# Kernel tuning notes

Hardware: AMD Instinct MI355X
Metric: run time of the kernel (lower is better)

## Reference

```python
import jax, jax.numpy as jnp
import numpy as np

B, S, L, E, H, T, V, D = 32, 256, 24, 300, 256, 16, 50000, 256  # batch, sents, words/sent, emb, gru_units, topics, vocab, dense


def setup_inputs() -> dict:
    key = jax.random.key(0)
    ks = jax.random.split(key, 12)
    word_ids = jax.random.randint(ks[0], (B, S, L), 0, V, dtype=jnp.int32)
    tsize = S // T
    starts = (jnp.arange(T, dtype=jnp.int32) * tsize + 1)          # 1-indexed inclusive
    ends = (jnp.arange(T, dtype=jnp.int32) * tsize + tsize)
    topic_start_ends = jnp.broadcast_to(jnp.stack([starts, ends], -1)[None], (B, T, 2))
    g = lambda k, shape, sc=0.05: (jax.random.normal(k, shape, jnp.float32) * sc)
    return {
        "word_ids": word_ids,
        "topic_start_ends": topic_start_ends,
        "emb": g(ks[1], (V, E), 0.1),
        "Wih_f": g(ks[2], (3 * H, E)), "Whh_f": g(ks[3], (3 * H, H)),
        "bih_f": jnp.zeros((3 * H,), jnp.float32), "bhh_f": jnp.zeros((3 * H,), jnp.float32),
        "Wih_b": g(ks[4], (3 * H, E)), "Whh_b": g(ks[5], (3 * H, H)),
        "bih_b": jnp.zeros((3 * H,), jnp.float32), "bhh_b": jnp.zeros((3 * H,), jnp.float32),
        "W_att": g(ks[6], (4 * H, 4 * H)), "v_att": g(ks[7], (4 * H, 1)),
        "W_dna": g(ks[8], (4 * H, D)), "b_dna": jnp.zeros((D,), jnp.float32),
        "W_out": g(ks[9], (D, 1)), "b_out": jnp.zeros((1,), jnp.float32),
    }


def _gru_dir(x, Wih, Whh, bih, bhh, reverse):
    # x: [B, S, E] -> outputs [B, S, H], final hidden [B, H]  (PyTorch GRU cell math)
    def step(h, xt):
        gi = xt @ Wih.T + bih
        gh = h @ Whh.T + bhh
        ir, iz, inn = jnp.split(gi, 3, axis=-1)
        hr, hz, hn = jnp.split(gh, 3, axis=-1)
        r = jax.nn.sigmoid(ir + hr)
        z = jax.nn.sigmoid(iz + hz)
        n = jnp.tanh(inn + r * hn)
        h2 = (1.0 - z) * n + z * h
        return h2, h2
    h0 = jnp.zeros((x.shape[0], Whh.shape[1]), x.dtype)
    hT, ys = jax.lax.scan(step, h0, jnp.swapaxes(x, 0, 1), reverse=reverse)
    return jnp.swapaxes(ys, 0, 1), hT


def _gather_seq(x, idx):
    # x: [B, S', C], idx: [B, K] -> [B, K, C]
    return jnp.take_along_axis(x, idx[:, :, None].astype(jnp.int32), axis=1)


def reference(word_ids, topic_start_ends, emb, Wih_f, Whh_f, bih_f, bhh_f,
              Wih_b, Whh_b, bih_b, bhh_b, W_att, v_att, W_dna, b_dna, W_out, b_out):
    # --- sent_encoder: per-sentence mean of word embeddings ---
    sent_vecs = jnp.mean(emb[word_ids], axis=2)  # [B, S, E]

    # --- doc_encoder: bidirectional GRU ---
    out_f, hT_f = _gru_dir(sent_vecs, Wih_f, Whh_f, bih_f, bhh_f, reverse=False)
    out_b, hT_b = _gru_dir(sent_vecs, Wih_b, Whh_b, bih_b, bhh_b, reverse=True)
    sent_rep = jnp.concatenate([out_f, out_b], axis=-1)          # [B, S, 2H]
    hidden = jnp.stack([hT_f, hT_b], axis=0)                     # [2, B, H]
    # faithful to torch: hidden.view(batch_size, 2H) (row-major reshape)
    doc_vec = hidden.reshape(B, 2 * H)
    doc_rep = jnp.broadcast_to(doc_vec[:, None, :], (B, S, 2 * H))

    # --- topic representation via boundary differencing on front/back-padded output ---
    padded = jnp.pad(sent_rep, ((0, 0), (1, 1), (0, 0)))         # [B, S+2, 2H]
    starts = topic_start_ends[..., 0]                            # [B, T], 1-indexed
    ends = topic_start_ends[..., 1]
    topic_fwd = _gather_seq(padded, ends)[..., :H] - _gather_seq(padded, starts - 1)[..., :H]
    topic_bwd = _gather_seq(padded, starts)[..., H:] - _gather_seq(padded, ends + 1)[..., H:]
    topic_mat = jnp.concatenate([topic_fwd, topic_bwd], axis=-1)  # [B, T, 2H]
    # sentence s (0-indexed) -> topic t with starts[t] <= s+1 <= ends[t]
    sent_1idx = jnp.arange(1, S + 1, dtype=jnp.int32)
    topic_id = jax.vmap(lambda e: jnp.searchsorted(e, sent_1idx, side='left'))(ends)  # [B, S]
    topic_rep = jnp.take_along_axis(topic_mat, topic_id[:, :, None], axis=1)          # [B, S, 2H]

    # --- decoder_attention ---
    cat_ds = jnp.concatenate([doc_rep, sent_rep], axis=-1)       # [B, S, 4H]
    cat_ts = jnp.concatenate([topic_rep, sent_rep], axis=-1)
    doc_scores = jnp.tanh(cat_ds @ W_att) @ v_att                # [B, S, 1]
    topic_scores = jnp.tanh(cat_ts @ W_att) @ v_att
    doc_w = jax.nn.softmax(doc_scores, axis=1)
    topic_w = jax.nn.softmax(topic_scores, axis=1)
    context = doc_w * doc_rep + topic_w * topic_rep              # [B, S, 2H]
    inp = jnp.concatenate([sent_rep, context], axis=-1)          # [B, S, 4H]
    h = jax.nn.relu(inp @ W_dna + b_dna)                         # dropout is identity (eval)
    logits = (h @ W_out + b_out)[..., 0]                         # [B, S]
    return logits
```

## Files before the change

kernel.cpp:

```cpp
#include <hip/hip_runtime.h>
#include <hip/hip_bf16.h>
#include <math.h>

#define Bd 32
#define Sd 256
#define Ld 24
#define Ed 300
#define Hd 256
#define Td 16
#define Dd 256
#define EP 320

using short8 = __attribute__((ext_vector_type(8))) short;
using f32x4  = __attribute__((ext_vector_type(4))) float;

__device__ __forceinline__ float fsigm(float x) { return 1.f / (1.f + __expf(-x)); }
__device__ __forceinline__ float ftanh(float x) {
  float e = __expf(2.f * x);
  return 1.f - 2.f / (e + 1.f);
}

__global__ void sent_means_kernel(const int* __restrict__ wids,
                                  const float* __restrict__ emb,
                                  __hip_bfloat16* __restrict__ apad) {
  int r = blockIdx.x;
  __shared__ int ids[Ld];
  int tid = threadIdx.x;
  if (tid < Ld) ids[tid] = wids[r * Ld + tid];
  __syncthreads();
  float acc = 0.f;
  if (tid < Ed) {
#pragma unroll
    for (int w = 0; w < Ld; ++w) acc += emb[(size_t)ids[w] * Ed + tid];
    acc *= (1.f / 24.f);
  }
  apad[r * EP + tid] = __float2bfloat16(tid < Ed ? acc : 0.f);
}

__global__ void prep1_kernel(const float* __restrict__ wih_f, const float* __restrict__ wih_b,
                             const float* __restrict__ whh_f, const float* __restrict__ whh_b,
                             __hip_bfloat16* __restrict__ wpadf, __hip_bfloat16* __restrict__ wpadb,
                             __hip_bfloat16* __restrict__ whhbf_f, __hip_bfloat16* __restrict__ whhbf_b) {
  int i = blockIdx.x * 512 + threadIdx.x;
  const int PW = 768 * EP;
  const int WH = 768 * Hd;
  if (i < 2 * PW) {
    const float* src = (i < PW) ? wih_f : wih_b;
    __hip_bfloat16* dst = (i < PW) ? wpadf : wpadb;
    int j = (i < PW) ? i : i - PW;
    int n = j / EP, k = j % EP;
    dst[j] = __float2bfloat16(k < Ed ? src[n * Ed + k] : 0.f);
  } else {
    int j = i - 2 * PW;
    const float* src = (j < WH) ? whh_f : whh_b;
    __hip_bfloat16* dst = (j < WH) ? whhbf_f : whhbf_b;
    int k = (j < WH) ? j : j - WH;
    dst[k] = __float2bfloat16(src[k]);
  }
}

__global__ __launch_bounds__(256) void gemm_xwt_kernel(
    const __hip_bfloat16* __restrict__ A, int lda,
    const __hip_bfloat16* __restrict__ W, int ldw,
    float* __restrict__ C, int ldc,
    int M, int N, int K,
    const float* __restrict__ bias) {
  __shared__ unsigned short la[64][32];
  __shared__ unsigned short lb[64][32];
  const int tid = threadIdx.x;
  const int m0 = blockIdx.x * 64, n0 = blockIdx.y * 64;
  const int lane = tid & 63, wid = tid >> 6;
  const int wm = (wid >> 1) * 32, wn = (wid & 1) * 32;
  const int lrow = tid >> 2, lcol = (tid & 3) * 8;
  f32x4 acc00 = {0.f, 0.f, 0.f, 0.f}, acc01 = {0.f, 0.f, 0.f, 0.f};
  f32x4 acc10 = {0.f, 0.f, 0.f, 0.f}, acc11 = {0.f, 0.f, 0.f, 0.f};
  int arow = m0 + lrow; if (arow > M - 1) arow = M - 1;
  const int brow = n0 + lrow;
  const int fr = lane & 15, fq = (lane >> 4) * 8;
  for (int k0 = 0; k0 < K; k0 += 32) {
    uint4 av = *(const uint4*)(A + (size_t)arow * lda + k0 + lcol);
    uint4 bv = *(const uint4*)(W + (size_t)brow * ldw + k0 + lcol);
    *(uint4*)(&la[lrow][lcol]) = av;
    *(uint4*)(&lb[lrow][lcol]) = bv;
    __syncthreads();
    short8 a0 = *(const short8*)(&la[wm + fr][fq]);
    short8 a1 = *(const short8*)(&la[wm + 16 + fr][fq]);
    short8 b0 = *(const short8*)(&lb[wn + fr][fq]);
    short8 b1 = *(const short8*)(&lb[wn + 16 + fr][fq]);
    acc00 = __builtin_amdgcn_mfma_f32_16x16x32_bf16(a0, b0, acc00, 0, 0, 0);
    acc01 = __builtin_amdgcn_mfma_f32_16x16x32_bf16(a0, b1, acc01, 0, 0, 0);
    acc10 = __builtin_amdgcn_mfma_f32_16x16x32_bf16(a1, b0, acc10, 0, 0, 0);
    acc11 = __builtin_amdgcn_mfma_f32_16x16x32_bf16(a1, b1, acc11, 0, 0, 0);
    __syncthreads();
  }
  const int rq = (lane >> 4) * 4;
  f32x4 accs[2][2] = {{acc00, acc01}, {acc10, acc11}};
  for (int i = 0; i < 2; ++i)
    for (int j = 0; j < 2; ++j) {
      int n = n0 + wn + j * 16 + fr;
      float bv = bias ? bias[n] : 0.f;
      for (int r2 = 0; r2 < 4; ++r2) {
        int m = m0 + wm + i * 16 + rq + r2;
        if (m < M) C[(size_t)m * ldc + n] = accs[i][j][r2] + bv;
      }
    }
}

__global__ __launch_bounds__(512, 2) void gru_mfma_kernel(
    const float* __restrict__ gi_f, const float* __restrict__ gi_b,
    const __hip_bfloat16* __restrict__ whhbf_f, const __hip_bfloat16* __restrict__ whhbf_b,
    const float* __restrict__ bhh_f, const float* __restrict__ bhh_b,
    float* __restrict__ sent_rep, __hip_bfloat16* __restrict__ sent_rep_bf,
    float* __restrict__ hT_f, float* __restrict__ hT_b,
    const float* __restrict__ w_att, const float* __restrict__ w_dna,
    __hip_bfloat16* __restrict__ wpack1, __hip_bfloat16* __restrict__ wpack2) {
  __shared__ float gi_lds[2][8][768];
  __shared__ __hip_bfloat16 h_bf[256];
  __shared__ float gh[768];
  __shared__ float stg32[8][256];
  const int blk = blockIdx.x;
  const int tid = threadIdx.x;

  if (blk >= 64) {
    const size_t q = (size_t)(blk - 64) * 512 + tid;
    size_t flat = q * 8;
    const size_t HALF = (size_t)1280 * 512;
    const bool second = flat >= HALF;
    size_t r = second ? flat - HALF : flat;
    int n = (int)(r >> 9), k0 = (int)(r & 511);
    __hip_bfloat16* dst = second ? wpack2 : wpack1;
#pragma unroll
    for (int j = 0; j < 8; ++j) {
      int k = k0 + j;
      float v;
      if (!second)
        v = (n < 1024) ? w_att[(size_t)k * 1024 + n]
                       : w_dna[(size_t)(512 + k) * 256 + (n - 1024)];
      else
        v = (n < 1024) ? w_att[(size_t)(512 + k) * 1024 + n]
                       : w_dna[(size_t)k * 256 + (n - 1024)];
      dst[(size_t)n * 512 + k] = __float2bfloat16(v);
    }
    return;
  }

  const int dir = blk >> 5, b = blk & 31;
  const int lane = tid & 63, w = tid >> 6;
  const float* gi = dir ? gi_b : gi_f;
  const __hip_bfloat16* whh = dir ? whhbf_b : whhbf_f;
  const float* bhh = dir ? bhh_b : bhh_f;

  if (tid < 256) h_bf[tid] = __float2bfloat16(0.f);

  short8 bfrag[6][8];
  {
    const int n0 = w * 96 + (lane & 15);
    const int kq = (lane >> 4) * 8;
#pragma unroll
    for (int nt = 0; nt < 6; ++nt)
#pragma unroll
      for (int kt = 0; kt < 8; ++kt)
        bfrag[nt][kt] = *(const short8*)(whh + (size_t)(n0 + nt * 16) * 256 + kt * 32 + kq);
  }
  float bhr = 0.f, bhz = 0.f, bhn = 0.f, hprev = 0.f;
  if (tid < 256) { bhr = bhh[tid]; bhz = bhh[256 + tid]; bhn = bhh[512 + tid]; }

  auto burst = [&](int tstart, int buf) {
#pragma unroll
    for (int i = 0; i < 3; ++i) {
      int idx = tid + i * 512;
      int u = idx / 192;
      int c4 = (idx - u * 192) * 4;
      int s = dir ? (255 - (tstart + u)) : (tstart + u);
      float4 v = *(const float4*)(gi + (size_t)(((b << 8) + s) * 768 + c4));
      *(float4*)(&gi_lds[buf][u][c4]) = v;
    }
  };
  burst(0, 0);
  __syncthreads();

  const int c = lane & 15;
  const int kq = (lane >> 4) * 8;
  const short8 zero8 = {0, 0, 0, 0, 0, 0, 0, 0};

  for (int t = 0; t < Sd; ++t) {
    if ((t & 7) == 0 && t + 8 < Sd) burst(t + 8, ((t >> 3) + 1) & 1);
    f32x4 acc[6];
#pragma unroll
    for (int nt = 0; nt < 6; ++nt) acc[nt] = (f32x4){0.f, 0.f, 0.f, 0.f};
#pragma unroll
    for (int kt = 0; kt < 8; ++kt) {
      short8 av = *(const short8*)(&h_bf[kt * 32 + kq]);
      if (c != 0) av = zero8;
#pragma unroll
      for (int nt = 0; nt < 6; ++nt)
        acc[nt] = __builtin_amdgcn_mfma_f32_16x16x32_bf16(av, bfrag[nt][kt], acc[nt], 0, 0, 0);
    }
    if (lane < 16) {
#pragma unroll
      for (int nt = 0; nt < 6; ++nt)
        gh[w * 96 + nt * 16 + lane] = acc[nt][0];
    }
    __syncthreads();
    if (tid < 256) {
      const float* gl = gi_lds[(t >> 3) & 1][t & 7];
      float rr = fsigm(gl[tid] + gh[tid] + bhr);
      float zz = fsigm(gl[256 + tid] + gh[256 + tid] + bhz);
      float nn = ftanh(gl[512 + tid] + rr * (gh[512 + tid] + bhn));
      float hn = (1.f - zz) * nn + zz * hprev;
      hprev = hn;
      h_bf[tid] = __float2bfloat16(hn);
      stg32[t & 7][tid] = hn;
    }
    __syncthreads();
    if ((t & 7) == 7) {
      const int base = t - 7;
#pragma unroll
      for (int i = 0; i < 4; ++i) {
        int idx = tid + i * 512;
        int u = idx >> 8, d = idx & 255;
        int sg = dir ? (255 - (base + u)) : (base + u);
        size_t rowg = (size_t)((b << 8) + sg);
        int col = dir ? (256 + d) : d;
        float v = stg32[u][d];
        sent_rep[rowg * 512 + col] = v;
        sent_rep_bf[rowg * 512 + col] = __float2bfloat16(v);
      }
    }
  }
  if (tid < 256) (dir ? hT_b : hT_f)[b * 256 + tid] = hprev;
}

__global__ void docvec_kernel(const float* __restrict__ hTf, const float* __restrict__ hTb,
                              __hip_bfloat16* __restrict__ dv) {
  int b = blockIdx.x, jj = threadIdx.x;
  int idx = b * 512 + jj;
  int dsel = idx >> 13;
  int rem = idx & 8191;
  int bp = rem >> 8, hp = rem & 255;
  float v = (dsel ? hTb : hTf)[bp * Hd + hp];
  dv[idx] = __float2bfloat16(v);
}

__global__ void topic_kernel(const int* __restrict__ tse, const float* __restrict__ sent_rep,
                             __hip_bfloat16* __restrict__ topic_bf) {
  int bt = blockIdx.x;
  int b = bt >> 4;
  int st = tse[bt * 2], en = tse[bt * 2 + 1];
  int dd = threadIdx.x;
  auto pad = [&](int i, int col) -> float {
    if (i < 1 || i > Sd) return 0.f;
    return sent_rep[((size_t)((b << 8) + (i - 1))) * 512 + col];
  };
  float fwd = pad(en, dd) - pad(st - 1, dd);
  float bwd = pad(st, Hd + dd) - pad(en + 1, Hd + dd);
  topic_bf[(size_t)bt * 512 + dd] = __float2bfloat16(fwd);
  topic_bf[(size_t)bt * 512 + Hd + dd] = __float2bfloat16(bwd);
}

__global__ void scores_kernel(const float* __restrict__ PD, const float* __restrict__ RT,
                              const float* __restrict__ QU, const float* __restrict__ v_att,
                              const int* __restrict__ tse,
                              float* __restrict__ dsc, float* __restrict__ tsc) {
  int r = blockIdx.x;
  int b = r >> 8, s = r & 255;
  int tid = threadIdx.x;
  int tsel = Td - 1;
  for (int t = 0; t < Td; ++t) {
    if (tse[(b * Td + t) * 2 + 1] >= s + 1) { tsel = t; break; }
  }
  const float* q = QU + (size_t)r * 1280;
  const float* p = PD + (size_t)b * 1280;
  const float* rr = RT + (size_t)(b * Td + tsel) * 1280;
  float accd = 0.f, acct = 0.f;
  for (int n = tid; n < 1024; n += 256) {
    float qv = q[n];
    float vv = v_att[n];
    accd += ftanh(p[n] + qv) * vv;
    acct += ftanh(rr[n] + qv) * vv;
  }
  __shared__ float s1[256], s2[256];
  s1[tid] = accd; s2[tid] = acct;
  __syncthreads();
  for (int off = 128; off > 0; off >>= 1) {
    if (tid < off) { s1[tid] += s1[tid + off]; s2[tid] += s2[tid + off]; }
    __syncthreads();
  }
  if (tid == 0) { dsc[r] = s1[0]; tsc[r] = s2[0]; }
}

__global__ void softmax_kernel(const float* __restrict__ dsc, const float* __restrict__ tsc,
                               float* __restrict__ dw, float* __restrict__ tw) {
  int b = blockIdx.x, s = threadIdx.x;
  __shared__ float red[256];
  for (int which = 0; which < 2; ++which) {
    const float* src = which ? tsc : dsc;
    float v = src[b * Sd + s];
    red[s] = v; __syncthreads();
    for (int off = 128; off > 0; off >>= 1) {
      if (s < off) red[s] = fmaxf(red[s], red[s + off]);
      __syncthreads();
    }
    float m = red[0]; __syncthreads();
    float e = __expf(v - m);
    red[s] = e; __syncthreads();
    for (int off = 128; off > 0; off >>= 1) {
      if (s < off) red[s] += red[s + off];
      __syncthreads();
    }
    float sum = red[0]; __syncthreads();
    (which ? tw : dw)[b * Sd + s] = e / sum;
  }
}

__global__ void final_kernel(const float* __restrict__ QU, const float* __restrict__ PD,
                             const float* __restrict__ RT, const float* __restrict__ dw,
                             const float* __restrict__ tw, const float* __restrict__ b_dna,
                             const float* __restrict__ w_out,
                             const float* __restrict__ b_out,
                             const int* __restrict__ tse, float* __restrict__ out) {
  int r = blockIdx.x;
  int b = r >> 8, s = r & 255;
  int dd = threadIdx.x;
  int tsel = Td - 1;
  for (int t = 0; t < Td; ++t) {
    if (tse[(b * Td + t) * 2 + 1] >= s + 1) { tsel = t; break; }
  }
  float wdv = dw[b * Sd + s], wtv = tw[b * Sd + s];
  float x = QU[(size_t)r * 1280 + 1024 + dd] + wdv * PD[(size_t)b * 1280 + 1024 + dd] +
            wtv * RT[(size_t)(b * Td + tsel) * 1280 + 1024 + dd] + b_dna[dd];
  x = fmaxf(x, 0.f);
  float term = x * w_out[dd];
  __shared__ float red[256];
  red[dd] = term; __syncthreads();
  for (int off = 128; off > 0; off >>= 1) {
    if (dd < off) red[dd] += red[dd + off];
    __syncthreads();
  }
  if (dd == 0) out[r] = red[0] + b_out[0];
}

static void launch_gemm(const __hip_bfloat16* A, int lda, const __hip_bfloat16* W, int ldw,
                        float* C, int ldc, int M, int N, int K,
                        const float* bias, hipStream_t stream) {
  dim3 grid((M + 63) / 64, N / 64);
  gemm_xwt_kernel<<<grid, 256, 0, stream>>>(A, lda, W, ldw, C, ldc, M, N, K, bias);
}

extern "C" void kernel_launch(void* const* d_in, const int* in_sizes, int n_in,
                              void* d_out, int out_size, void* d_ws, size_t ws_size,
                              hipStream_t stream) {
  const int* word_ids = (const int*)d_in[0];
  const int* tse      = (const int*)d_in[1];
  const float* emb   = (const float*)d_in[2];
  const float* wih_f = (const float*)d_in[3];
  const float* whh_f = (const float*)d_in[4];
  const float* bih_f = (const float*)d_in[5];
  const float* bhh_f = (const float*)d_in[6];
  const float* wih_b = (const float*)d_in[7];
  const float* whh_b = (const float*)d_in[8];
  const float* bih_b = (const float*)d_in[9];
  const float* bhh_b = (const float*)d_in[10];
  const float* w_att = (const float*)d_in[11];
  const float* v_att = (const float*)d_in[12];
  const float* w_dna = (const float*)d_in[13];
  const float* b_dna = (const float*)d_in[14];
  const float* w_out = (const float*)d_in[15];
  const float* b_out = (const float*)d_in[16];
  float* out = (float*)d_out;
  char* ws = (char*)d_ws;

  const int M = Bd * Sd;

  size_t off = 0;
  auto alloc = [&](size_t sz) { size_t o = off; off += (sz + 255) & ~(size_t)255; return o; };
  size_t o_svbf   = alloc((size_t)M * EP * 2);
  size_t o_wpadf  = alloc((size_t)768 * EP * 2);
  size_t o_wpadb  = alloc((size_t)768 * EP * 2);
  size_t o_whhbf  = alloc((size_t)768 * Hd * 2 * 2);
  size_t o_wpack1 = alloc((size_t)1280 * 512 * 2);
  size_t o_wpack2 = alloc((size_t)1280 * 512 * 2);
  size_t o_hTf    = alloc((size_t)Bd * Hd * 4);
  size_t o_hTb    = alloc((size_t)Bd * Hd * 4);
  size_t o_dvbf   = alloc((size_t)Bd * 512 * 2);
  size_t o_topbf  = alloc((size_t)Bd * Td * 512 * 2);
  size_t o_PD     = alloc((size_t)Bd * 1280 * 4);
  size_t o_RT     = alloc((size_t)Bd * Td * 1280 * 4);
  size_t o_dsc    = alloc((size_t)Bd * Sd * 4);
  size_t o_tsc    = alloc((size_t)Bd * Sd * 4);
  size_t o_dw     = alloc((size_t)Bd * Sd * 4);
  size_t o_tw     = alloc((size_t)Bd * Sd * 4);
  size_t o_srep32 = alloc((size_t)M * 512 * 4);
  size_t o_srepbf = alloc((size_t)M * 512 * 2);
  size_t o_gif    = alloc((size_t)M * 768 * 4);
  size_t o_gib    = alloc((size_t)M * 768 * 4);
  size_t o_QU = o_gif;
  (void)ws_size;

  __hip_bfloat16* svbf   = (__hip_bfloat16*)(ws + o_svbf);
  __hip_bfloat16* wpadf  = (__hip_bfloat16*)(ws + o_wpadf);
  __hip_bfloat16* wpadb  = (__hip_bfloat16*)(ws + o_wpadb);
  __hip_bfloat16* whhbf_f = (__hip_bfloat16*)(ws + o_whhbf);
  __hip_bfloat16* whhbf_b = whhbf_f + 768 * Hd;
  __hip_bfloat16* wpack1 = (__hip_bfloat16*)(ws + o_wpack1);
  __hip_bfloat16* wpack2 = (__hip_bfloat16*)(ws + o_wpack2);
  float* hTf = (float*)(ws + o_hTf);
  float* hTb = (float*)(ws + o_hTb);
  __hip_bfloat16* dvbf  = (__hip_bfloat16*)(ws + o_dvbf);
  __hip_bfloat16* topbf = (__hip_bfloat16*)(ws + o_topbf);
  float* PD  = (float*)(ws + o_PD);
  float* RT  = (float*)(ws + o_RT);
  float* dsc = (float*)(ws + o_dsc);
  float* tsc = (float*)(ws + o_tsc);
  float* dw  = (float*)(ws + o_dw);
  float* tw  = (float*)(ws + o_tw);
  float* srep32 = (float*)(ws + o_srep32);
  __hip_bfloat16* srepbf = (__hip_bfloat16*)(ws + o_srepbf);
  float* gif = (float*)(ws + o_gif);
  float* gib = (float*)(ws + o_gib);
  float* QU  = (float*)(ws + o_QU);

  sent_means_kernel<<<M, EP, 0, stream>>>(word_ids, emb, svbf);
  prep1_kernel<<<1728, 512, 0, stream>>>(wih_f, wih_b, whh_f, whh_b,
                                         wpadf, wpadb, whhbf_f, whhbf_b);
  launch_gemm(svbf, EP, wpadf, EP, gif, 768, M, 768, EP, bih_f, stream);
  launch_gemm(svbf, EP, wpadb, EP, gib, 768, M, 768, EP, bih_b, stream);
  gru_mfma_kernel<<<384, 512, 0, stream>>>(gif, gib, whhbf_f, whhbf_b, bhh_f, bhh_b,
                                           srep32, srepbf, hTf, hTb,
                                           w_att, w_dna, wpack1, wpack2);
  docvec_kernel<<<Bd, 512, 0, stream>>>(hTf, hTb, dvbf);
  topic_kernel<<<Bd * Td, 256, 0, stream>>>(tse, srep32, topbf);
  launch_gemm(srepbf, 512, wpack2, 512, QU, 1280, M, 1280, 512, nullptr, stream);
  launch_gemm(dvbf, 512, wpack1, 512, PD, 1280, Bd, 1280, 512, nullptr, stream);
  launch_gemm(topbf, 512, wpack1, 512, RT, 1280, Bd * Td, 1280, 512, nullptr, stream);
  scores_kernel<<<M, 256, 0, stream>>>(PD, RT, QU, v_att, tse, dsc, tsc);
  softmax_kernel<<<Bd, 256, 0, stream>>>(dsc, tsc, dw, tw);
  final_kernel<<<M, 256, 0, stream>>>(QU, PD, RT, dw, tw, b_dna, w_out, b_out, tse, out);
}
```

Before: 581.5 us.

## Remap GRU gate columns per wave to drop gh LDS exchange and a barrier

Each wave now owns the r/z/n gate columns for the same 32 hidden units, so it computes the gate nonlinearity straight from its MFMA accumulators. This removes the gh shared-memory round trip and one of the two barriers per timestep. The hidden state is double-buffered in LDS, and the gi prefetch uses global_load_lds direct-to-LDS copies with hand-placed waitcnt/barrier asm. Only 16 lanes per wave do the elementwise work, so that phase has less parallelism, and the hand-written synchronisation is fragile.

```diff
diff --git a/kernel.cpp b/kernel.cpp
--- a/kernel.cpp
+++ b/kernel.cpp
@@ -115,8 +115,7 @@
     const float* __restrict__ w_att, const float* __restrict__ w_dna,
     __hip_bfloat16* __restrict__ wpack1, __hip_bfloat16* __restrict__ wpack2) {
   __shared__ float gi_lds[2][8][768];
-  __shared__ __hip_bfloat16 h_bf[256];
-  __shared__ float gh[768];
+  __shared__ __hip_bfloat16 h_bf[2][256];
   __shared__ float stg32[8][256];
   const int blk = blockIdx.x;
   const int tid = threadIdx.x;
@@ -150,20 +149,8 @@
   const __hip_bfloat16* whh = dir ? whhbf_b : whhbf_f;
   const float* bhh = dir ? bhh_b : bhh_f;
 
-  if (tid < 256) h_bf[tid] = __float2bfloat16(0.f);
-
-  short8 bfrag[6][8];
-  {
-    const int n0 = w * 96 + (lane & 15);
-    const int kq = (lane >> 4) * 8;
-#pragma unroll
-    for (int nt = 0; nt < 6; ++nt)
-#pragma unroll
-      for (int kt = 0; kt < 8; ++kt)
-        bfrag[nt][kt] = *(const short8*)(whh + (size_t)(n0 + nt * 16) * 256 + kt * 32 + kq);
-  }
-  float bhr = 0.f, bhz = 0.f, bhn = 0.f, hprev = 0.f;
-  if (tid < 256) { bhr = bhh[tid]; bhz = bhh[256 + tid]; bhn = bhh[512 + tid]; }
+  const int fr = lane & 15;
+  const int kq = (lane >> 4) * 8;
 
   auto burst = [&](int tstart, int buf) {
 #pragma unroll
@@ -172,48 +159,76 @@
       int u = idx / 192;
       int c4 = (idx - u * 192) * 4;
       int s = dir ? (255 - (tstart + u)) : (tstart + u);
-      float4 v = *(const float4*)(gi + (size_t)(((b << 8) + s) * 768 + c4));
-      *(float4*)(&gi_lds[buf][u][c4]) = v;
+      const float* g = gi + (size_t)(((b << 8) + s) * 768 + c4);
+      float* l = &gi_lds[buf][u][c4];
+      __builtin_amdgcn_global_load_lds(
+          (const __attribute__((address_space(1))) unsigned int*)g,
+          (__attribute__((address_space(3))) unsigned int*)l, 16, 0, 0);
     }
   };
   burst(0, 0);
-  __syncthreads();
-
-  const int c = lane & 15;
-  const int kq = (lane >> 4) * 8;
-  const short8 zero8 = {0, 0, 0, 0, 0, 0, 0, 0};
+
+  if (tid < 256) h_bf[0][tid] = __float2bfloat16(0.f);
+
+  short8 bfrag[6][8];
+  {
+#pragma unroll
+    for (int g = 0; g < 3; ++g)
+#pragma unroll
+      for (int half = 0; half < 2; ++half)
+#pragma unroll
+        for (int kt = 0; kt < 8; ++kt)
+          bfrag[g * 2 + half][kt] =
+              *(const short8*)(whh + (size_t)(g * 256 + w * 32 + half * 16 + fr) * 256 +
+                               kt * 32 + kq);
+  }
+
+  const int j1 = w * 32 + lane;
+  const int j2 = j1 + 16;
+  float bhr1 = 0.f, bhz1 = 0.f, bhn1 = 0.f, hp1 = 0.f;
+  float bhr2 = 0.f, bhz2 = 0.f, bhn2 = 0.f, hp2 = 0.f;
+  if (lane < 16) {
+    bhr1 = bhh[j1]; bhz1 = bhh[256 + j1]; bhn1 = bhh[512 + j1];
+    bhr2 = bhh[j2]; bhz2 = bhh[256 + j2]; bhn2 = bhh[512 + j2];
+  }
+
+  asm volatile("s_waitcnt vmcnt(0) lgkmcnt(0)\n\ts_barrier" ::: "memory");
 
   for (int t = 0; t < Sd; ++t) {
     if ((t & 7) == 0 && t + 8 < Sd) burst(t + 8, ((t >> 3) + 1) & 1);
+    const int rb = t & 1, wb = rb ^ 1;
+
     f32x4 acc[6];
 #pragma unroll
     for (int nt = 0; nt < 6; ++nt) acc[nt] = (f32x4){0.f, 0.f, 0.f, 0.f};
 #pragma unroll
     for (int kt = 0; kt < 8; ++kt) {
-      short8 av = *(const short8*)(&h_bf[kt * 32 + kq]);
-      if (c != 0) av = zero8;
+      short8 av = *(const short8*)(&h_bf[rb][kt * 32 + kq]);
 #pragma unroll
       for (int nt = 0; nt < 6; ++nt)
         acc[nt] = __builtin_amdgcn_mfma_f32_16x16x32_bf16(av, bfrag[nt][kt], acc[nt], 0, 0, 0);
     }
+
     if (lane < 16) {
-#pragma unroll
-      for (int nt = 0; nt < 6; ++nt)
-        gh[w * 96 + nt * 16 + lane] = acc[nt][0];
-    }
-    __syncthreads();
-    if (tid < 256) {
       const float* gl = gi_lds[(t >> 3) & 1][t & 7];
-      float rr = fsigm(gl[tid] + gh[tid] + bhr);
-      float zz = fsigm(gl[256 + tid] + gh[256 + tid] + bhz);
-      float nn = ftanh(gl[512 + tid] + rr * (gh[512 + tid] + bhn));
-      float hn = (1.f - zz) * nn + zz * hprev;
-      hprev = hn;
-      h_bf[tid] = __float2bfloat16(hn);
-      stg32[t & 7][tid] = hn;
-    }
-    __syncthreads();
+      float r1 = fsigm(gl[j1] + acc[0][0] + bhr1);
+      float z1 = fsigm(gl[256 + j1] + acc[2][0] + bhz1);
+      float n1 = ftanh(gl[512 + j1] + r1 * (acc[4][0] + bhn1));
+      float h1 = (1.f - z1) * n1 + z1 * hp1;
+      hp1 = h1;
+      float r2 = fsigm(gl[j2] + acc[1][0] + bhr2);
+      float z2 = fsigm(gl[256 + j2] + acc[3][0] + bhz2);
+      float n2 = ftanh(gl[512 + j2] + r2 * (acc[5][0] + bhn2));
+      float h2 = (1.f - z2) * n2 + z2 * hp2;
+      hp2 = h2;
+      h_bf[wb][j1] = __float2bfloat16(h1);
+      h_bf[wb][j2] = __float2bfloat16(h2);
+      stg32[t & 7][j1] = h1;
+      stg32[t & 7][j2] = h2;
+    }
+
     if ((t & 7) == 7) {
+      asm volatile("s_waitcnt vmcnt(0) lgkmcnt(0)\n\ts_barrier" ::: "memory");
       const int base = t - 7;
 #pragma unroll
       for (int i = 0; i < 4; ++i) {
@@ -226,9 +241,16 @@
         sent_rep[rowg * 512 + col] = v;
         sent_rep_bf[rowg * 512 + col] = __float2bfloat16(v);
       }
-    }
-  }
-  if (tid < 256) (dir ? hT_b : hT_f)[b * 256 + tid] = hprev;
+      asm volatile("s_waitcnt lgkmcnt(0)\n\ts_barrier" ::: "memory");
+    } else {
+      asm volatile("s_waitcnt lgkmcnt(0)\n\ts_barrier" ::: "memory");
+    }
+  }
+  if (lane < 16) {
+    float* hT = dir ? hT_b : hT_f;
+    hT[b * 256 + j1] = hp1;
+    hT[b * 256 + j2] = hp2;
+  }
 }
 
 __global__ void docvec_kernel(const float* __restrict__ hTf, const float* __restrict__ hTb,
```

New measurement: 633.4 us. 1.09x slower.

## Pipeline GRU recurrence with async LDS loads and warp-specialized output writes

Applied to the files above, without the earlier changes.

Restructures the per-step GRU loop. The upper 256 threads issue the gi prefetch with global_load_lds direct-to-LDS loads and write back sentence outputs one 8-step group late, so the 256 gate-math threads never stall on them. The hidden state and the staging buffers are double-buffered, and the zeroing select on the A fragment is dropped. Raw s_waitcnt/s_barrier asm replaces __syncthreads, and the launch bound drops to one block per SIMD group, allowing more registers. The explicit wait counts must be exactly right, or the code will read stale data.

```diff
diff --git a/kernel.cpp b/kernel.cpp
--- a/kernel.cpp
+++ b/kernel.cpp
@@ -106,7 +106,7 @@
     }
 }
 
-__global__ __launch_bounds__(512, 2) void gru_mfma_kernel(
+__global__ __launch_bounds__(512, 1) void gru_mfma_kernel(
     const float* __restrict__ gi_f, const float* __restrict__ gi_b,
     const __hip_bfloat16* __restrict__ whhbf_f, const __hip_bfloat16* __restrict__ whhbf_b,
     const float* __restrict__ bhh_f, const float* __restrict__ bhh_b,
@@ -115,9 +115,9 @@
     const float* __restrict__ w_att, const float* __restrict__ w_dna,
     __hip_bfloat16* __restrict__ wpack1, __hip_bfloat16* __restrict__ wpack2) {
   __shared__ float gi_lds[2][8][768];
-  __shared__ __hip_bfloat16 h_bf[256];
+  __shared__ __hip_bfloat16 h_bf[2][256];
   __shared__ float gh[768];
-  __shared__ float stg32[8][256];
+  __shared__ float stg32[2][8][256];
   const int blk = blockIdx.x;
   const int tid = threadIdx.x;
 
@@ -150,58 +150,58 @@
   const __hip_bfloat16* whh = dir ? whhbf_b : whhbf_f;
   const float* bhh = dir ? bhh_b : bhh_f;
 
-  if (tid < 256) h_bf[tid] = __float2bfloat16(0.f);
-
-  short8 bfrag[6][8];
   {
-    const int n0 = w * 96 + (lane & 15);
-    const int kq = (lane >> 4) * 8;
-#pragma unroll
-    for (int nt = 0; nt < 6; ++nt)
-#pragma unroll
-      for (int kt = 0; kt < 8; ++kt)
-        bfrag[nt][kt] = *(const short8*)(whh + (size_t)(n0 + nt * 16) * 256 + kt * 32 + kq);
-  }
-  float bhr = 0.f, bhz = 0.f, bhn = 0.f, hprev = 0.f;
-  if (tid < 256) { bhr = bhh[tid]; bhz = bhh[256 + tid]; bhn = bhh[512 + tid]; }
-
-  auto burst = [&](int tstart, int buf) {
 #pragma unroll
     for (int i = 0; i < 3; ++i) {
       int idx = tid + i * 512;
       int u = idx / 192;
       int c4 = (idx - u * 192) * 4;
-      int s = dir ? (255 - (tstart + u)) : (tstart + u);
-      float4 v = *(const float4*)(gi + (size_t)(((b << 8) + s) * 768 + c4));
-      *(float4*)(&gi_lds[buf][u][c4]) = v;
-    }
-  };
-  burst(0, 0);
-  __syncthreads();
-
-  const int c = lane & 15;
-  const int kq = (lane >> 4) * 8;
-  const short8 zero8 = {0, 0, 0, 0, 0, 0, 0, 0};
+      int s = dir ? (255 - u) : u;
+      const float* g = gi + (size_t)(((b << 8) + s) * 768 + c4);
+      __builtin_amdgcn_global_load_lds(
+          (const __attribute__((address_space(1))) unsigned int*)g,
+          (__attribute__((address_space(3))) unsigned int*)&gi_lds[0][u][c4], 16, 0, 0);
+    }
+  }
+  if (tid < 256) h_bf[0][tid] = __float2bfloat16(0.f);
+
+  const int fr = lane & 15, kq = (lane >> 4) * 8;
+  short8 bfrag[6][8];
+  {
+    const int n0 = w * 96 + fr;
+#pragma unroll
+    for (int nt = 0; nt < 6; ++nt)
+#pragma unroll
+      for (int kt = 0; kt < 8; ++kt)
+        bfrag[nt][kt] = *(const short8*)(whh + (size_t)(n0 + nt * 16) * 256 + kt * 32 + kq);
+  }
+
+  float bhr = 0.f, bhz = 0.f, bhn = 0.f, hprev = 0.f;
+  if (tid < 256) { bhr = bhh[tid]; bhz = bhh[256 + tid]; bhn = bhh[512 + tid]; }
+
+  asm volatile("s_waitcnt vmcnt(0) lgkmcnt(0)\n\ts_barrier" ::: "memory");
 
   for (int t = 0; t < Sd; ++t) {
-    if ((t & 7) == 0 && t + 8 < Sd) burst(t + 8, ((t >> 3) + 1) & 1);
+    const int rb = t & 1, wb = rb ^ 1;
+
     f32x4 acc[6];
 #pragma unroll
     for (int nt = 0; nt < 6; ++nt) acc[nt] = (f32x4){0.f, 0.f, 0.f, 0.f};
 #pragma unroll
     for (int kt = 0; kt < 8; ++kt) {
-      short8 av = *(const short8*)(&h_bf[kt * 32 + kq]);
-      if (c != 0) av = zero8;
+      short8 av = *(const short8*)(&h_bf[rb][kt * 32 + kq]);
 #pragma unroll
       for (int nt = 0; nt < 6; ++nt)
         acc[nt] = __builtin_amdgcn_mfma_f32_16x16x32_bf16(av, bfrag[nt][kt], acc[nt], 0, 0, 0);
     }
     if (lane < 16) {
 #pragma unroll
-      for (int nt = 0; nt < 6; ++nt)
-        gh[w * 96 + nt * 16 + lane] = acc[nt][0];
-    }
-    __syncthreads();
+      for (int nt = 0; nt < 6; ++nt) gh[w * 96 + nt * 16 + lane] = acc[nt][0];
+    }
+    if (w >= 4 && (t & 7) == 0)
+      asm volatile("s_waitcnt vmcnt(0)" ::: "memory");
+    asm volatile("s_waitcnt lgkmcnt(0)\n\ts_barrier" ::: "memory");
+
     if (tid < 256) {
       const float* gl = gi_lds[(t >> 3) & 1][t & 7];
       float rr = fsigm(gl[tid] + gh[tid] + bhr);
@@ -209,26 +209,55 @@
       float nn = ftanh(gl[512 + tid] + rr * (gh[512 + tid] + bhn));
       float hn = (1.f - zz) * nn + zz * hprev;
       hprev = hn;
-      h_bf[tid] = __float2bfloat16(hn);
-      stg32[t & 7][tid] = hn;
-    }
-    __syncthreads();
-    if ((t & 7) == 7) {
-      const int base = t - 7;
-#pragma unroll
-      for (int i = 0; i < 4; ++i) {
-        int idx = tid + i * 512;
-        int u = idx >> 8, d = idx & 255;
-        int sg = dir ? (255 - (base + u)) : (base + u);
-        size_t rowg = (size_t)((b << 8) + sg);
-        int col = dir ? (256 + d) : d;
-        float v = stg32[u][d];
-        sent_rep[rowg * 512 + col] = v;
-        sent_rep_bf[rowg * 512 + col] = __float2bfloat16(v);
+      h_bf[wb][tid] = __float2bfloat16(hn);
+      stg32[(t >> 3) & 1][t & 7][tid] = hn;
+    } else if ((t & 7) == 0) {
+      if (t + 8 < Sd) {
+        const int buf = ((t >> 3) + 1) & 1;
+#pragma unroll
+        for (int i = 0; i < 6; ++i) {
+          int idx = (tid - 256) + i * 256;
+          int u = idx / 192;
+          int c4 = (idx - u * 192) * 4;
+          int s = dir ? (255 - (t + 8 + u)) : (t + 8 + u);
+          const float* g = gi + (size_t)(((b << 8) + s) * 768 + c4);
+          __builtin_amdgcn_global_load_lds(
+              (const __attribute__((address_space(1))) unsigned int*)g,
+              (__attribute__((address_space(3))) unsigned int*)&gi_lds[buf][u][c4], 16, 0, 0);
+        }
       }
-    }
-  }
-  if (tid < 256) (dir ? hT_b : hT_f)[b * 256 + tid] = hprev;
+      if (t >= 8) {
+        const int base = t - 8;
+        const int gp = ((t >> 3) - 1) & 1;
+        const int d = tid - 256;
+#pragma unroll
+        for (int u = 0; u < 8; ++u) {
+          int sg = dir ? (255 - (base + u)) : (base + u);
+          size_t rowg = (size_t)((b << 8) + sg);
+          int col = dir ? (256 + d) : d;
+          float v = stg32[gp][u][d];
+          sent_rep[rowg * 512 + col] = v;
+          sent_rep_bf[rowg * 512 + col] = __float2bfloat16(v);
+        }
+      }
+    }
+    asm volatile("s_waitcnt lgkmcnt(0)\n\ts_barrier" ::: "memory");
+  }
+
+  if (w >= 4) {
+    const int base = 248, d = tid - 256;
+#pragma unroll
+    for (int u = 0; u < 8; ++u) {
+      int sg = dir ? (255 - (base + u)) : (base + u);
+      size_t rowg = (size_t)((b << 8) + sg);
+      int col = dir ? (256 + d) : d;
+      float v = stg32[1][u][d];
+      sent_rep[rowg * 512 + col] = v;
+      sent_rep_bf[rowg * 512 + col] = __float2bfloat16(v);
+    }
+  } else {
+    (dir ? hT_b : hT_f)[b * 256 + tid] = hprev;
+  }
 }
 
 __global__ void docvec_kernel(const float* __restrict__ hTf, const float* __restrict__ hTb,
```

Result: no change. 577.0 us (-0.8%).
